# Kernel optimization log

Hardware: AMD Instinct MI355X
Metric: run time of the kernel (lower is better)

The kernel has to match this reference:

```python
import jax, jax.numpy as jnp
import numpy as np
import math

L = 4      # layers / experts
AD = 512   # agent dim per layer
D = 512    # wsi_size / model dim
T = 64     # num_tokens
N = 4096   # WSI patches
NC = 2
PROJ = 256 # cosine gate projection dim
HID = 4 * D
CAP = math.ceil(T / L)  # top-1, capacity_factor=1.0
EPS = 1e-5
AUX_W = 0.01


def layer_norm(x, g, b):
    x32 = x.astype(jnp.float32)
    mu = x32.mean(-1, keepdims=True)
    var = x32.var(-1, keepdims=True)
    return ((x32 - mu) * jax.lax.rsqrt(var + EPS) * g + b).astype(x.dtype)


def mha(q_in, kv_in, w_qkv, b_qkv, w_out, b_out, n_heads):
    # torch nn.MultiheadAttention, unbatched (len, embed) inputs
    E = q_in.shape[-1]
    hd = E // n_heads
    wq, wk, wv = jnp.split(w_qkv, 3, axis=0)
    bq, bk, bv = jnp.split(b_qkv, 3)
    q = (q_in @ wq.T + bq).reshape(-1, n_heads, hd)
    k = (kv_in @ wk.T + bk).reshape(-1, n_heads, hd)
    v = (kv_in @ wv.T + bv).reshape(-1, n_heads, hd)
    scale = float(1.0 / np.sqrt(hd))
    attn = jax.nn.softmax(jnp.einsum('thd,shd->hts', q, k) * scale, axis=-1)
    out = jnp.einsum('hts,shd->thd', attn, v).reshape(-1, E)
    return out @ w_out.T + b_out


def moe_top1(x, proj_w, sim_mat, temp, w1, b1, w2, b2):
    # tutel cosine top-1 gate (fp32), capacity-limited batch-prioritized dispatch
    E = w1.shape[0]
    xf = x.astype(jnp.float32)
    p = xf @ proj_w                                             # [T, PROJ]
    p = p / (jnp.linalg.norm(p, axis=-1, keepdims=True) + 1e-8)
    s = sim_mat / (jnp.linalg.norm(sim_mat, axis=0, keepdims=True) + 1e-8)
    scale = jnp.exp(jnp.minimum(temp, jnp.log(jnp.float32(100.0))))
    logits = (p @ s) * scale                                    # [T, E]
    scores = jax.nn.softmax(logits, axis=-1)
    expert = jnp.argmax(logits, axis=-1)                        # [T]
    gate = jnp.take_along_axis(scores, expert[:, None], axis=1)[:, 0]
    # batch prioritized routing: higher-gate tokens claim capacity slots first
    order = jnp.argsort(-gate)
    oh = jax.nn.one_hot(expert[order], E, dtype=jnp.int32)
    pos_s = jnp.sum(jnp.cumsum(oh, axis=0) * oh, axis=1) - 1    # slot within expert
    inv = jnp.argsort(order)
    pos = pos_s[inv]
    keep = pos < CAP
    safe_pos = jnp.where(keep, pos, 0)
    # dispatch -> grouped expert FFN -> combine
    buf = jnp.zeros((E, CAP, x.shape[-1]), x.dtype)
    buf = buf.at[expert, safe_pos].add(jnp.where(keep[:, None], x, 0.0))
    h = jax.nn.gelu(jnp.einsum('ecd,edh->ech', buf, w1) + b1[:, None, :], approximate=False)
    y = jnp.einsum('ech,ehd->ecd', h, w2) + b2[:, None, :]
    out = y[expert, safe_pos] * (gate * keep)[:, None].astype(x.dtype)
    # load-balancing aux loss (top-1)
    me = scores.mean(0)
    ce = jax.nn.one_hot(expert, E, dtype=jnp.float32).mean(0)
    l_aux = jnp.sum(me * ce) * E
    return out, l_aux


def reference(share_feature, fet_tokens, ind_ln1_g, ind_ln1_b, ind_ln2_g, ind_ln2_b,
              ind_qkv_w, ind_qkv_b, ind_out_w, ind_out_b, ind_mlp_w, ind_mlp_b,
              gate_proj_w, gate_sim, gate_temp, exp_w1, exp_b1, exp_w2, exp_b2,
              gsa_ln1_g, gsa_ln1_b, gsa_qkv_w, gsa_qkv_b, gsa_out_w, gsa_out_b,
              gsa_ln2_g, gsa_ln2_b, gsa_fc_w, gsa_fc_b, gsa_proj_w, gsa_proj_b,
              butter_w, butter_b, cls_w, cls_b):
    cur = jnp.zeros((T, D), share_feature.dtype)
    feature1 = jnp.zeros((L, T, D), share_feature.dtype)
    aux = jnp.zeros((1,), jnp.float32)
    for i in range(L):  # small fixed per-layer loop (structurally distinct params)
        seg = share_feature[:, i * AD:(i + 1) * AD]
        sf = layer_norm(seg, ind_ln1_g[i], ind_ln1_b[i])
        tok = layer_norm(fet_tokens[i], ind_ln2_g[i], ind_ln2_b[i])
        attn_out = mha(tok, sf, ind_qkv_w[i], ind_qkv_b[i], ind_out_w[i], ind_out_b[i], AD)
        qf = attn_out @ ind_mlp_w[i].T + ind_mlp_b[i]   # [T, D]
        mo, la = moe_top1(qf, gate_proj_w, gate_sim, gate_temp, exp_w1, exp_b1, exp_w2, exp_b2)
        cur = cur + mo
        aux = aux + la * AUX_W
        feature1 = feature1.at[i].set(cur)
    cur = cur / L
    # GatedSFAttentionBlock (8 heads self-attn + QuickGELU MLP, pre-LN residual)
    x1 = layer_norm(cur, gsa_ln1_g, gsa_ln1_b)
    x = cur + mha(x1, x1, gsa_qkv_w, gsa_qkv_b, gsa_out_w, gsa_out_b, D // 64)
    x2 = layer_norm(x, gsa_ln2_g, gsa_ln2_b)
    h = x2 @ gsa_fc_w.T + gsa_fc_b
    h = h * jax.nn.sigmoid(1.702 * h)  # QuickGELU
    gated = x + (h @ gsa_proj_w.T + gsa_proj_b)
    # OutputBlock
    hb = (gated @ butter_w.T + butter_b).reshape(1, -1)  # [1, T*256]
    logits = hb @ cls_w.T + cls_b                        # [1, NC]
    Y_hat = jnp.argmax(logits, axis=1, keepdims=True)
    hazards = jax.nn.sigmoid(logits)
    feature2 = jnp.zeros((L, T, D), share_feature.dtype)
    feature2_pre = jnp.zeros((L, 1, NC), share_feature.dtype)
    return (logits, hazards, Y_hat, aux, feature1, feature2, feature2_pre)


def setup_inputs() -> dict:
    key = jax.random.key(0)
    ks = iter(jax.random.split(key, 40))
    def rn(shape, scale=0.02):
        return scale * jax.random.normal(next(ks), shape, dtype=jnp.float32)
    return dict(
        share_feature=jax.random.normal(next(ks), (N, L * AD), dtype=jnp.float32),
        fet_tokens=rn((L, T, AD), AD ** -0.5),
        ind_ln1_g=jnp.ones((L, AD)), ind_ln1_b=jnp.zeros((L, AD)),
        ind_ln2_g=jnp.ones((L, AD)), ind_ln2_b=jnp.zeros((L, AD)),
        ind_qkv_w=rn((L, 3 * AD, AD)), ind_qkv_b=jnp.zeros((L, 3 * AD)),
        ind_out_w=rn((L, AD, AD)), ind_out_b=jnp.zeros((L, AD)),
        ind_mlp_w=rn((L, D, AD)), ind_mlp_b=jnp.zeros((L, D)),
        gate_proj_w=rn((D, PROJ)), gate_sim=rn((PROJ, L)),
        gate_temp=jnp.asarray(np.log(10.0), jnp.float32),
        exp_w1=rn((L, D, HID)), exp_b1=jnp.zeros((L, HID)),
        exp_w2=rn((L, HID, D)), exp_b2=jnp.zeros((L, D)),
        gsa_ln1_g=jnp.ones((D,)), gsa_ln1_b=jnp.zeros((D,)),
        gsa_qkv_w=rn((3 * D, D)), gsa_qkv_b=jnp.zeros((3 * D,)),
        gsa_out_w=rn((D, D)), gsa_out_b=jnp.zeros((D,)),
        gsa_ln2_g=jnp.ones((D,)), gsa_ln2_b=jnp.zeros((D,)),
        gsa_fc_w=rn((4 * D, D)), gsa_fc_b=jnp.zeros((4 * D,)),
        gsa_proj_w=rn((D, 4 * D)), gsa_proj_b=jnp.zeros((D,)),
        butter_w=rn((256, D)), butter_b=jnp.zeros((256,)),
        cls_w=rn((NC, T * 256)), cls_b=jnp.zeros((NC,)),
    )
```

## Files before the change

### kernel.cpp

```cpp
#include <hip/hip_runtime.h>
#include <math.h>

#define LNUM 4
#define ADIM 512
#define TTOK 64
#define NSEQ 4096
#define HIDE 2048
#define CAPE 16
#define EPSV 1e-5f

typedef __bf16 bf16;
typedef bf16 bf16x8 __attribute__((ext_vector_type(8)));
typedef float f32x4 __attribute__((ext_vector_type(4)));

#define OFF_KT      0
#define OFF_VT      (OFF_KT   + LNUM*512*NSEQ)
#define OFF_KMAX    (OFF_VT   + LNUM*512*NSEQ)
#define OFF_KMIN    (OFF_KMAX + LNUM*512)
#define OFF_Q       (OFF_KMIN + LNUM*512)
#define OFF_AO      (OFF_Q    + LNUM*TTOK*512)
#define OFF_AP      (OFF_AO   + LNUM*TTOK*512)
#define OFF_QF      (OFF_AP   + LNUM*TTOK*512)
#define OFF_GATE    (OFF_QF   + LNUM*TTOK*512)
#define OFF_EXP     (OFF_GATE + LNUM*TTOK)
#define OFF_POS     (OFF_EXP  + LNUM*TTOK)
#define OFF_KEEP    (OFF_POS  + LNUM*TTOK)
#define OFF_BUF     (OFF_KEEP + LNUM*TTOK)
#define OFF_SSUM    (OFF_BUF  + LNUM*4*CAPE*512)
#define OFF_CNT     (OFF_SSUM + LNUM*4)
#define ZERO_N      (LNUM*4*CAPE*512 + LNUM*4 + LNUM*4)
#define OFF_HEXP    (OFF_CNT  + LNUM*4)
#define OFF_YEXP    (OFF_HEXP + LNUM*4*CAPE*HIDE)
#define OFF_CUR     (OFF_YEXP + LNUM*4*CAPE*512)
#define OFF_Q3      (OFF_CUR  + TTOK*512)
#define OFF_K3      (OFF_Q3   + TTOK*512)
#define OFF_V3      (OFF_K3   + TTOK*512)
#define OFF_AO2     (OFF_V3   + TTOK*512)
#define OFF_XB      (OFF_AO2  + TTOK*512)
#define OFF_HROW    (OFF_XB   + TTOK*512)
#define OFF_HB      (OFF_HROW + TTOK*HIDE)
#define OFF_GATED   (OFF_HB   + TTOK*256)
#define OFF_AH      (OFF_GATED + TTOK*512)
#define OFF_AL      (OFF_AH + LNUM*NSEQ*256)
#define OFF_WH      (OFF_AL + LNUM*NSEQ*256)
#define OFF_WL      (OFF_WH + LNUM*1024*256)

#define O_F1   6
#define O_F2   (6 + LNUM*TTOK*512)
#define O_F2P  (O_F2 + LNUM*TTOK*512)

__device__ __forceinline__ float wave_sum(float v) {
#pragma unroll
  for (int o = 32; o > 0; o >>= 1) v += __shfl_down(v, o, 64);
  return v;
}

__device__ __forceinline__ float block_sum256(float v) {
  __shared__ float r[4];
  v = wave_sum(v);
  int wid = threadIdx.x >> 6, lane = threadIdx.x & 63;
  if (lane == 0) r[wid] = v;
  __syncthreads();
  float s = r[0] + r[1] + r[2] + r[3];
  __syncthreads();
  return s;
}

__global__ void k_zero(float* __restrict__ p, int n) {
  int i = blockIdx.x * 256 + threadIdx.x;
  if (i < n) p[i] = 0.f;
}

__global__ __launch_bounds__(64) void k_cvt_a(const float* __restrict__ SF,
      const float* __restrict__ G, const float* __restrict__ Bta,
      bf16* __restrict__ AH, bf16* __restrict__ AL) {
  int row = blockIdx.x;
  int l = row >> 12, m = row & 4095;
  int lane = threadIdx.x;
  const float* src = SF + (size_t)m * (LNUM * ADIM) + l * ADIM;
  float4 a = *(const float4*)(src + lane * 8);
  float4 b = *(const float4*)(src + lane * 8 + 4);
  float sum = (a.x + a.y) + (a.z + a.w) + (b.x + b.y) + (b.z + b.w);
  float sq = a.x*a.x + a.y*a.y + a.z*a.z + a.w*a.w + b.x*b.x + b.y*b.y + b.z*b.z + b.w*b.w;
  sum = wave_sum(sum); sq = wave_sum(sq);
  sum = __shfl(sum, 0, 64); sq = __shfl(sq, 0, 64);
  float mu = sum * (1.f / 512.f);
  float rs = rsqrtf(sq * (1.f / 512.f) - mu * mu + EPSV);
  float4 g0 = *(const float4*)(G + l * 512 + lane * 8);
  float4 g1 = *(const float4*)(G + l * 512 + lane * 8 + 4);
  float4 c0 = *(const float4*)(Bta + l * 512 + lane * 8);
  float4 c1 = *(const float4*)(Bta + l * 512 + lane * 8 + 4);
  float x[8];
  x[0] = (a.x - mu) * rs * g0.x + c0.x;  x[1] = (a.y - mu) * rs * g0.y + c0.y;
  x[2] = (a.z - mu) * rs * g0.z + c0.z;  x[3] = (a.w - mu) * rs * g0.w + c0.w;
  x[4] = (b.x - mu) * rs * g1.x + c1.x;  x[5] = (b.y - mu) * rs * g1.y + c1.y;
  x[6] = (b.z - mu) * rs * g1.z + c1.z;  x[7] = (b.w - mu) * rs * g1.w + c1.w;
  bf16x8 vh, vl;
#pragma unroll
  for (int j = 0; j < 8; j++) {
    bf16 h = (bf16)x[j];
    vh[j] = h;
    vl[j] = (bf16)(x[j] - (float)h);
  }
  *(bf16x8*)(AH + (size_t)row * 512 + lane * 8) = vh;
  *(bf16x8*)(AL + (size_t)row * 512 + lane * 8) = vl;
}

__global__ __launch_bounds__(64) void k_cvt_w(const float* __restrict__ Wqkv,
      bf16* __restrict__ WH, bf16* __restrict__ WL) {
  int row = blockIdx.x;
  int l = row >> 10, r = row & 1023;
  int lane = threadIdx.x;
  const float* src = Wqkv + (size_t)l * 1536 * 512 + (size_t)(512 + r) * 512 + lane * 8;
  float4 a = *(const float4*)(src);
  float4 b = *(const float4*)(src + 4);
  float x[8] = {a.x, a.y, a.z, a.w, b.x, b.y, b.z, b.w};
  bf16x8 vh, vl;
#pragma unroll
  for (int j = 0; j < 8; j++) {
    bf16 h = (bf16)x[j];
    vh[j] = h;
    vl[j] = (bf16)(x[j] - (float)h);
  }
  *(bf16x8*)(WH + (size_t)row * 512 + lane * 8) = vh;
  *(bf16x8*)(WL + (size_t)row * 512 + lane * 8) = vl;
}

__global__ __launch_bounds__(256) void k_mfma_kv(
      const bf16* __restrict__ AH, const bf16* __restrict__ AL,
      const bf16* __restrict__ WH, const bf16* __restrict__ WL,
      const float* __restrict__ Bqkv,
      float* __restrict__ KT, float* __restrict__ VT) {
  __shared__ bf16 sAh[128*32], sAl[128*32], sWh[128*32], sWl[128*32];
  int l = blockIdx.z;
  int n0 = blockIdx.x * 128, m0 = blockIdx.y * 128;
  int tid = threadIdx.x;
  int lane = tid & 63;
  int w = tid >> 6;
  int wm = w >> 1, wn = w & 1;
  const bf16* gAh = AH + ((size_t)l * 4096 + m0) * 512;
  const bf16* gAl = AL + ((size_t)l * 4096 + m0) * 512;
  const bf16* gWh = WH + ((size_t)l * 1024 + n0) * 512;
  const bf16* gWl = WL + ((size_t)l * 1024 + n0) * 512;
  int ch0 = tid * 2, ch1 = tid * 2 + 1;
  int r0 = ch0 >> 2, q0 = (ch0 & 3) * 8;
  int r1 = ch1 >> 2, q1 = (ch1 & 3) * 8;
  int fr = lane & 15, fq = (lane >> 4) * 8;
  f32x4 acc[4][4] = {};
  for (int k0 = 0; k0 < 512; k0 += 32) {
    *(bf16x8*)&sAh[r0*32 + q0] = *(const bf16x8*)&gAh[(size_t)r0*512 + k0 + q0];
    *(bf16x8*)&sAh[r1*32 + q1] = *(const bf16x8*)&gAh[(size_t)r1*512 + k0 + q1];
    *(bf16x8*)&sAl[r0*32 + q0] = *(const bf16x8*)&gAl[(size_t)r0*512 + k0 + q0];
    *(bf16x8*)&sAl[r1*32 + q1] = *(const bf16x8*)&gAl[(size_t)r1*512 + k0 + q1];
    *(bf16x8*)&sWh[r0*32 + q0] = *(const bf16x8*)&gWh[(size_t)r0*512 + k0 + q0];
    *(bf16x8*)&sWh[r1*32 + q1] = *(const bf16x8*)&gWh[(size_t)r1*512 + k0 + q1];
    *(bf16x8*)&sWl[r0*32 + q0] = *(const bf16x8*)&gWl[(size_t)r0*512 + k0 + q0];
    *(bf16x8*)&sWl[r1*32 + q1] = *(const bf16x8*)&gWl[(size_t)r1*512 + k0 + q1];
    __syncthreads();
    bf16x8 ah[4], al[4], bh[4], bl[4];
#pragma unroll
    for (int i = 0; i < 4; i++) {
      ah[i] = *(const bf16x8*)&sAh[(wm*64 + i*16 + fr)*32 + fq];
      al[i] = *(const bf16x8*)&sAl[(wm*64 + i*16 + fr)*32 + fq];
      bh[i] = *(const bf16x8*)&sWh[(wn*64 + i*16 + fr)*32 + fq];
      bl[i] = *(const bf16x8*)&sWl[(wn*64 + i*16 + fr)*32 + fq];
    }
#pragma unroll
    for (int i = 0; i < 4; i++)
#pragma unroll
      for (int j = 0; j < 4; j++) {
        acc[i][j] = __builtin_amdgcn_mfma_f32_16x16x32_bf16(ah[i], bh[j], acc[i][j], 0, 0, 0);
        acc[i][j] = __builtin_amdgcn_mfma_f32_16x16x32_bf16(ah[i], bl[j], acc[i][j], 0, 0, 0);
        acc[i][j] = __builtin_amdgcn_mfma_f32_16x16x32_bf16(al[i], bh[j], acc[i][j], 0, 0, 0);
      }
    __syncthreads();
  }
#pragma unroll
  for (int j = 0; j < 4; j++) {
    int n = n0 + wn*64 + j*16 + fr;
    float bias = Bqkv[l * 1536 + 512 + n];
    float* base = (n < 512) ? (KT + ((size_t)(l*512 + n)) * 4096)
                            : (VT + ((size_t)(l*512 + n - 512)) * 4096);
#pragma unroll
    for (int i = 0; i < 4; i++) {
      int mb = m0 + wm*64 + i*16 + (lane >> 4) * 4;
      float4 o = make_float4(acc[i][j][0] + bias, acc[i][j][1] + bias,
                             acc[i][j][2] + bias, acc[i][j][3] + bias);
      *(float4*)(base + mb) = o;
    }
  }
}

__global__ __launch_bounds__(256) void k_minmax(const float* __restrict__ KT,
                                                float* __restrict__ kmax, float* __restrict__ kmin) {
  int row = blockIdx.x;
  const float4* k = (const float4*)(KT + (size_t)row * 4096);
  float mx = -3.4e38f, mn = 3.4e38f;
  for (int i = threadIdx.x; i < 1024; i += 256) {
    float4 v = k[i];
    mx = fmaxf(mx, fmaxf(fmaxf(v.x, v.y), fmaxf(v.z, v.w)));
    mn = fminf(mn, fminf(fminf(v.x, v.y), fminf(v.z, v.w)));
  }
#pragma unroll
  for (int o = 32; o > 0; o >>= 1) {
    mx = fmaxf(mx, __shfl_down(mx, o, 64));
    mn = fminf(mn, __shfl_down(mn, o, 64));
  }
  __shared__ float rmx[4], rmn[4];
  int wid = threadIdx.x >> 6, lane = threadIdx.x & 63;
  if (lane == 0) { rmx[wid] = mx; rmn[wid] = mn; }
  __syncthreads();
  if (threadIdx.x == 0) {
    kmax[row] = fmaxf(fmaxf(rmx[0], rmx[1]), fmaxf(rmx[2], rmx[3]));
    kmin[row] = fminf(fminf(rmn[0], rmn[1]), fminf(rmn[2], rmn[3]));
  }
}

__global__ __launch_bounds__(256) void k_q(const float* __restrict__ TOK,
      const float* __restrict__ G, const float* __restrict__ Bta,
      const float* __restrict__ Wqkv, const float* __restrict__ Bqkv,
      float* __restrict__ Q) {
  int t = blockIdx.x, l = blockIdx.y;
  int tid = threadIdx.x;
  __shared__ float xr[512];
  const float* x = TOK + ((size_t)l * TTOK + t) * ADIM;
  float v0 = x[tid], v1 = x[tid + 256];
  float sum = block_sum256(v0 + v1);
  float sq = block_sum256(v0 * v0 + v1 * v1);
  float m = sum * (1.f / 512.f);
  float rs = rsqrtf(sq * (1.f / 512.f) - m * m + EPSV);
  xr[tid]       = (v0 - m) * rs * G[l * 512 + tid] + Bta[l * 512 + tid];
  xr[tid + 256] = (v1 - m) * rs * G[l * 512 + tid + 256] + Bta[l * 512 + tid + 256];
  __syncthreads();
  int h = blockIdx.z * 256 + tid;
  const float4* w = (const float4*)(Wqkv + (size_t)l * 1536 * 512 + (size_t)h * 512);
  float acc = 0.f;
#pragma unroll 8
  for (int c = 0; c < 128; c++) {
    float4 wv = w[c]; float4 xv = ((const float4*)xr)[c];
    acc = fmaf(wv.x, xv.x, acc); acc = fmaf(wv.y, xv.y, acc);
    acc = fmaf(wv.z, xv.z, acc); acc = fmaf(wv.w, xv.w, acc);
  }
  Q[((size_t)l * TTOK + t) * 512 + h] = acc + Bqkv[l * 1536 + h];
}

__global__ __launch_bounds__(256) void k_attn(const float* __restrict__ KT, const float* __restrict__ VT,
      const float* __restrict__ Q, const float* __restrict__ kmax, const float* __restrict__ kmin,
      float* __restrict__ AO) {
  int h = blockIdx.x, l = blockIdx.y;
  int tid = threadIdx.x;
  int w = tid >> 6, lane = tid & 63;
  __shared__ float pden[4][64], pnum[4][64];
  size_t base = ((size_t)(l * 512 + h)) * 4096 + w * 1024;
  float kv[16], vv[16];
#pragma unroll
  for (int c = 0; c < 4; c++) {
    *(float4*)&kv[c*4] = *(const float4*)(KT + base + c * 256 + lane * 4);
    *(float4*)&vv[c*4] = *(const float4*)(VT + base + c * 256 + lane * 4);
  }
  float q_own = Q[((size_t)l * TTOK + lane) * 512 + h];
  float km = kmax[l * 512 + h], kn = kmin[l * 512 + h];
  for (int t = 0; t < 64; t++) {
    float qt = __shfl(q_own, t, 64);
    float mt = (qt >= 0.f) ? qt * km : qt * kn;
    float den = 0.f, num = 0.f;
#pragma unroll
    for (int i = 0; i < 16; i++) {
      float e = __expf(fmaf(qt, kv[i], -mt));
      den += e;
      num = fmaf(e, vv[i], num);
    }
#pragma unroll
    for (int o = 32; o > 0; o >>= 1) {
      den += __shfl_down(den, o, 64);
      num += __shfl_down(num, o, 64);
    }
    if (lane == 0) { pden[w][t] = den; pnum[w][t] = num; }
  }
  __syncthreads();
  if (w == 0) {
    float d = pden[0][lane] + pden[1][lane] + pden[2][lane] + pden[3][lane];
    float n = pnum[0][lane] + pnum[1][lane] + pnum[2][lane] + pnum[3][lane];
    AO[((size_t)l * TTOK + lane) * 512 + h] = n / d;
  }
}

__global__ __launch_bounds__(256) void k_rowgemm512(const float* __restrict__ IN,
      const float* __restrict__ W, const float* __restrict__ B, const float* __restrict__ RES,
      float* __restrict__ OUT, unsigned long long wsl, int bsl) {
  int t = blockIdx.x, l = blockIdx.y;
  int row = l * gridDim.x + t;
  int tid = threadIdx.x;
  const float4* xr = (const float4*)(IN + (size_t)row * 512);
  int h = blockIdx.z * 256 + tid;
  const float4* w = (const float4*)(W + (size_t)l * wsl + (size_t)h * 512);
  float acc = 0.f;
#pragma unroll 8
  for (int c = 0; c < 128; c++) {
    float4 wv = w[c]; float4 xv = xr[c];
    acc = fmaf(wv.x, xv.x, acc); acc = fmaf(wv.y, xv.y, acc);
    acc = fmaf(wv.z, xv.z, acc); acc = fmaf(wv.w, xv.w, acc);
  }
  float o = acc + B[l * bsl + h];
  if (RES) o += RES[(size_t)row * 512 + h];
  OUT[(size_t)row * 512 + h] = o;
}

__global__ __launch_bounds__(256) void k_gate(const float* __restrict__ QF,
      const float* __restrict__ PW, const float* __restrict__ SIM, const float* __restrict__ TEMP,
      float* __restrict__ gate, int* __restrict__ expert,
      float* __restrict__ ssum, int* __restrict__ cnt) {
  int t = blockIdx.x, l = blockIdx.y;
  int tid = threadIdx.x;
  __shared__ float sp[256];
  __shared__ float lg[4];
  const float* x = QF + ((size_t)l * TTOK + t) * 512;
  float p = 0.f;
  for (int c = 0; c < 512; c++) p = fmaf(x[c], PW[c * 256 + tid], p);
  float nrm = block_sum256(p * p);
  float pn = p / (sqrtf(nrm) + 1e-8f);
  sp[tid] = pn;
  __syncthreads();
  if (tid < 4) {
    float ls = 0.f, ns = 0.f;
    for (int j = 0; j < 256; j++) {
      float sv = SIM[j * 4 + tid];
      ls = fmaf(sp[j], sv, ls);
      ns = fmaf(sv, sv, ns);
    }
    float scale = __expf(fminf(TEMP[0], 4.6051701859880914f));
    lg[tid] = ls / (sqrtf(ns) + 1e-8f) * scale;
  }
  __syncthreads();
  if (tid == 0) {
    float l0 = lg[0], l1 = lg[1], l2 = lg[2], l3 = lg[3];
    int best = 0; float bv = l0;
    if (l1 > bv) { best = 1; bv = l1; }
    if (l2 > bv) { best = 2; bv = l2; }
    if (l3 > bv) { best = 3; bv = l3; }
    float mx = fmaxf(fmaxf(l0, l1), fmaxf(l2, l3));
    float e0 = __expf(l0 - mx), e1 = __expf(l1 - mx), e2 = __expf(l2 - mx), e3 = __expf(l3 - mx);
    float inv = 1.f / (e0 + e1 + e2 + e3);
    float s0 = e0 * inv, s1 = e1 * inv, s2 = e2 * inv, s3 = e3 * inv;
    float sb = (best == 0) ? s0 : (best == 1) ? s1 : (best == 2) ? s2 : s3;
    gate[l * TTOK + t] = sb;
    expert[l * TTOK + t] = best;
    atomicAdd(&ssum[l * 4 + 0], s0); atomicAdd(&ssum[l * 4 + 1], s1);
    atomicAdd(&ssum[l * 4 + 2], s2); atomicAdd(&ssum[l * 4 + 3], s3);
    atomicAdd(&cnt[l * 4 + best], 1);
  }
}

__global__ __launch_bounds__(64) void k_route(const float* __restrict__ gate, const int* __restrict__ expert,
                                              int* __restrict__ pos, int* __restrict__ keep) {
  int l = blockIdx.x;
  int t = threadIdx.x;
  __shared__ float g[64];
  __shared__ int e[64];
  g[t] = gate[l * TTOK + t]; e[t] = expert[l * TTOK + t];
  __syncthreads();
  float gt = g[t]; int et = e[t];
  int p = 0;
  for (int u = 0; u < 64; u++)
    if (e[u] == et && (g[u] > gt || (g[u] == gt && u < t))) p++;
  pos[l * TTOK + t] = p;
  keep[l * TTOK + t] = (p < CAPE) ? 1 : 0;
}

__global__ __launch_bounds__(128) void k_scatter(const float* __restrict__ QF, const int* __restrict__ expert,
      const int* __restrict__ pos, const int* __restrict__ keep, float* __restrict__ buf) {
  int t = blockIdx.x, l = blockIdx.y;
  int idx = l * TTOK + t;
  if (!keep[idx]) return;
  int e = expert[idx], p = pos[idx];
  const float4* src = (const float4*)(QF + ((size_t)l * TTOK + t) * 512);
  float4* dst = (float4*)(buf + (((size_t)(l * 4 + e)) * CAPE + p) * 512);
  dst[threadIdx.x] = src[threadIdx.x];
}

__global__ __launch_bounds__(256) void k_moe_h(const float* __restrict__ buf, const float* __restrict__ W1,
      const float* __restrict__ B1, float* __restrict__ H) {
  int le = blockIdx.y;
  int e = le & 3;
  int col = blockIdx.x * 256 + threadIdx.x;
  const float* act = buf + (size_t)le * 16 * 512;
  const float* wp = W1 + (size_t)e * 512 * HIDE + col;
  float acc[16];
#pragma unroll
  for (int c = 0; c < 16; c++) acc[c] = 0.f;
  for (int k0 = 0; k0 < 512; k0 += 4) {
    float4 a[16];
#pragma unroll
    for (int c = 0; c < 16; c++) a[c] = *(const float4*)(act + c * 512 + k0);
#pragma unroll
    for (int j = 0; j < 4; j++) {
      float wv = wp[(size_t)(k0 + j) * HIDE];
#pragma unroll
      for (int c = 0; c < 16; c++) acc[c] = fmaf(((const float*)&a[c])[j], wv, acc[c]);
    }
  }
  float bias = B1[e * HIDE + col];
  float* outp = H + (size_t)le * 16 * HIDE + col;
#pragma unroll
  for (int c = 0; c < 16; c++) {
    float v = acc[c] + bias;
    outp[(size_t)c * HIDE] = 0.5f * v * (1.f + erff(v * 0.70710678118654752f));
  }
}

__global__ __launch_bounds__(256) void k_moe_y(const float* __restrict__ H, const float* __restrict__ W2,
      const float* __restrict__ B2, float* __restrict__ Y) {
  int le = blockIdx.y;
  int e = le & 3;
  int cl = threadIdx.x & 63, kq = threadIdx.x >> 6;
  int col = blockIdx.x * 64 + cl;
  const float* act = H + (size_t)le * 16 * HIDE + kq * 512;
  const float* wp = W2 + (size_t)e * HIDE * 512 + (size_t)(kq * 512) * 512 + col;
  float acc[16];
#pragma unroll
  for (int c = 0; c < 16; c++) acc[c] = 0.f;
  for (int k0 = 0; k0 < 512; k0 += 4) {
    float4 a[16];
#pragma unroll
    for (int c = 0; c < 16; c++) a[c] = *(const float4*)(act + c * HIDE + k0);
#pragma unroll
    for (int j = 0; j < 4; j++) {
      float wv = wp[(size_t)(k0 + j) * 512];
#pragma unroll
      for (int c = 0; c < 16; c++) acc[c] = fmaf(((const float*)&a[c])[j], wv, acc[c]);
    }
  }
  __shared__ float sacc[4][16][64];
#pragma unroll
  for (int c = 0; c < 16; c++) sacc[kq][c][cl] = acc[c];
  __syncthreads();
  if (kq == 0) {
    float bias = B2[e * 512 + col];
#pragma unroll
    for (int c = 0; c < 16; c++) {
      float tot = sacc[0][c][cl] + sacc[1][c][cl] + sacc[2][c][cl] + sacc[3][c][cl] + bias;
      Y[(size_t)le * 16 * 512 + (size_t)c * 512 + col] = tot;
    }
  }
}

__global__ __launch_bounds__(512) void k_combine(const float* __restrict__ Y, const int* __restrict__ expert,
      const int* __restrict__ pos, const int* __restrict__ keep, const float* __restrict__ gate,
      float* __restrict__ f1, float* __restrict__ f2, float* __restrict__ cur) {
  int t = blockIdx.x;
  int d = threadIdx.x;
  float acc = 0.f;
#pragma unroll
  for (int l = 0; l < LNUM; l++) {
    int idx = l * TTOK + t;
    float v = 0.f;
    if (keep[idx]) {
      int e = expert[idx], p = pos[idx];
      v = Y[(((size_t)(l * 4 + e)) * CAPE + p) * 512 + d] * gate[idx];
    }
    acc += v;
    f1[((size_t)l * TTOK + t) * 512 + d] = acc;
    f2[((size_t)l * TTOK + t) * 512 + d] = 0.f;
  }
  cur[(size_t)t * 512 + d] = acc * 0.25f;
}

__global__ __launch_bounds__(256) void k_gsa_qkv(const float* __restrict__ CUR,
      const float* __restrict__ G, const float* __restrict__ Bta,
      const float* __restrict__ W, const float* __restrict__ B,
      float* __restrict__ Q3, float* __restrict__ K3, float* __restrict__ V3) {
  int t = blockIdx.x;
  int tid = threadIdx.x;
  __shared__ float xr[512];
  const float* x = CUR + (size_t)t * 512;
  float v0 = x[tid], v1 = x[tid + 256];
  float sum = block_sum256(v0 + v1);
  float sq = block_sum256(v0 * v0 + v1 * v1);
  float m = sum * (1.f / 512.f);
  float rs = rsqrtf(sq * (1.f / 512.f) - m * m + EPSV);
  xr[tid] = (v0 - m) * rs * G[tid] + Bta[tid];
  xr[tid + 256] = (v1 - m) * rs * G[tid + 256] + Bta[tid + 256];
  __syncthreads();
  int h = blockIdx.y * 256 + tid;
  const float4* w = (const float4*)(W + (size_t)h * 512);
  float acc = 0.f;
#pragma unroll 8
  for (int c = 0; c < 128; c++) {
    float4 wv = w[c]; float4 xv = ((const float4*)xr)[c];
    acc = fmaf(wv.x, xv.x, acc); acc = fmaf(wv.y, xv.y, acc);
    acc = fmaf(wv.z, xv.z, acc); acc = fmaf(wv.w, xv.w, acc);
  }
  float o = acc + B[h];
  if (h < 512) Q3[(size_t)t * 512 + h] = o;
  else if (h < 1024) K3[(size_t)t * 512 + (h - 512)] = o;
  else V3[(size_t)t * 512 + (h - 1024)] = o;
}

__global__ __launch_bounds__(256) void k_gsa_attn(const float* __restrict__ Q3, const float* __restrict__ K3,
      const float* __restrict__ V3, float* __restrict__ AO2) {
  int h = blockIdx.x;
  __shared__ float qh[64][65], kh[64][65], vh[64][65];
  __shared__ float ps[4][64];
  for (int i = threadIdx.x; i < 4096; i += 256) {
    int t = i >> 6, d = i & 63;
    qh[t][d] = Q3[(size_t)t * 512 + h * 64 + d];
    kh[t][d] = K3[(size_t)t * 512 + h * 64 + d];
    vh[t][d] = V3[(size_t)t * 512 + h * 64 + d];
  }
  __syncthreads();
  int w = threadIdx.x >> 6, lane = threadIdx.x & 63;
  for (int tt = 0; tt < 16; tt++) {
    int t = w * 16 + tt;
    float acc = 0.f;
#pragma unroll 8
    for (int d = 0; d < 64; d++) acc = fmaf(qh[t][d], kh[lane][d], acc);
    acc *= 0.125f;
    float m = acc;
#pragma unroll
    for (int o = 32; o > 0; o >>= 1) m = fmaxf(m, __shfl_xor(m, o, 64));
    float e = __expf(acc - m);
    float den = e;
#pragma unroll
    for (int o = 32; o > 0; o >>= 1) den += __shfl_xor(den, o, 64);
    ps[w][lane] = e / den;
    __syncthreads();
    float o2 = 0.f;
#pragma unroll 8
    for (int s = 0; s < 64; s++) o2 = fmaf(ps[w][s], vh[s][lane], o2);
    AO2[(size_t)t * 512 + h * 64 + lane] = o2;
    __syncthreads();
  }
}

__global__ __launch_bounds__(256) void k_gsa_fc(const float* __restrict__ XB,
      const float* __restrict__ G, const float* __restrict__ Bta,
      const float* __restrict__ W, const float* __restrict__ B, float* __restrict__ H) {
  int t = blockIdx.x;
  int tid = threadIdx.x;
  __shared__ float xr[512];
  const float* x = XB + (size_t)t * 512;
  float v0 = x[tid], v1 = x[tid + 256];
  float sum = block_sum256(v0 + v1);
  float sq = block_sum256(v0 * v0 + v1 * v1);
  float m = sum * (1.f / 512.f);
  float rs = rsqrtf(sq * (1.f / 512.f) - m * m + EPSV);
  xr[tid] = (v0 - m) * rs * G[tid] + Bta[tid];
  xr[tid + 256] = (v1 - m) * rs * G[tid + 256] + Bta[tid + 256];
  __syncthreads();
  int o = blockIdx.y * 256 + tid;
  const float4* w = (const float4*)(W + (size_t)o * 512);
  float acc = 0.f;
#pragma unroll 8
  for (int c = 0; c < 128; c++) {
    float4 wv = w[c]; float4 xv = ((const float4*)xr)[c];
    acc = fmaf(wv.x, xv.x, acc); acc = fmaf(wv.y, xv.y, acc);
    acc = fmaf(wv.z, xv.z, acc); acc = fmaf(wv.w, xv.w, acc);
  }
  acc += B[o];
  H[(size_t)t * HIDE + o] = acc / (1.f + __expf(-1.702f * acc));
}

__global__ __launch_bounds__(256) void k_gsa_gated(const float* __restrict__ XB, const float* __restrict__ HROW,
      const float* __restrict__ PW, const float* __restrict__ PB, float* __restrict__ GATED) {
  int t = blockIdx.x;
  int tid = threadIdx.x;
  const float4* hp = (const float4*)(HROW + (size_t)t * HIDE);
  int o = blockIdx.y * 256 + tid;
  const float4* w = (const float4*)(PW + (size_t)o * HIDE);
  float acc = 0.f;
#pragma unroll 4
  for (int c = 0; c < 512; c++) {
    float4 wv = w[c]; float4 xv = hp[c];
    acc = fmaf(wv.x, xv.x, acc); acc = fmaf(wv.y, xv.y, acc);
    acc = fmaf(wv.z, xv.z, acc); acc = fmaf(wv.w, xv.w, acc);
  }
  GATED[(size_t)t * 512 + o] = acc + PB[o] + XB[(size_t)t * 512 + o];
}

__global__ __launch_bounds__(256) void k_butter(const float* __restrict__ GATED,
      const float* __restrict__ BW, const float* __restrict__ BB, float* __restrict__ HB) {
  int t = blockIdx.x;
  int tid = threadIdx.x;
  const float4* gr = (const float4*)(GATED + (size_t)t * 512);
  const float4* w = (const float4*)(BW + (size_t)tid * 512);
  float acc = 0.f;
#pragma unroll 8
  for (int c = 0; c < 128; c++) {
    float4 wv = w[c]; float4 xv = gr[c];
    acc = fmaf(wv.x, xv.x, acc); acc = fmaf(wv.y, xv.y, acc);
    acc = fmaf(wv.z, xv.z, acc); acc = fmaf(wv.w, xv.w, acc);
  }
  HB[(size_t)t * 256 + tid] = acc + BB[tid];
}

__global__ __launch_bounds__(256) void k_final(const float* __restrict__ HB,
      const float* __restrict__ CW, const float* __restrict__ CB,
      const float* __restrict__ ssum, const int* __restrict__ cnt,
      float* __restrict__ out) {
  int tid = threadIdx.x;
  float p0 = 0.f, p1 = 0.f;
  for (int i = tid; i < 16384; i += 256) {
    float h = HB[i];
    p0 = fmaf(h, CW[i], p0);
    p1 = fmaf(h, CW[16384 + i], p1);
  }
  p0 = block_sum256(p0);
  p1 = block_sum256(p1);
  if (tid == 0) {
    float l0 = p0 + CB[0], l1 = p1 + CB[1];
    out[0] = l0; out[1] = l1;
    out[2] = 1.f / (1.f + __expf(-l0));
    out[3] = 1.f / (1.f + __expf(-l1));
    out[4] = (l1 > l0) ? 1.f : 0.f;
    float aux = 0.f;
    for (int i = 0; i < 16; i++) aux += (ssum[i] * (1.f / 64.f)) * ((float)cnt[i] * (1.f / 64.f));
    out[5] = aux * 4.f * 0.01f;
  }
  if (tid < 8) out[O_F2P + tid] = 0.f;
}

extern "C" void kernel_launch(void* const* d_in, const int* in_sizes, int n_in,
                              void* d_out, int out_size, void* d_ws, size_t ws_size,
                              hipStream_t stream) {
  const float* SF    = (const float*)d_in[0];
  const float* TOK   = (const float*)d_in[1];
  const float* LN1G  = (const float*)d_in[2];
  const float* LN1B  = (const float*)d_in[3];
  const float* LN2G  = (const float*)d_in[4];
  const float* LN2B  = (const float*)d_in[5];
  const float* QKVW  = (const float*)d_in[6];
  const float* QKVB  = (const float*)d_in[7];
  const float* OUTW  = (const float*)d_in[8];
  const float* OUTB  = (const float*)d_in[9];
  const float* MLPW  = (const float*)d_in[10];
  const float* MLPB  = (const float*)d_in[11];
  const float* GPW   = (const float*)d_in[12];
  const float* GSIM  = (const float*)d_in[13];
  const float* GTMP  = (const float*)d_in[14];
  const float* EW1   = (const float*)d_in[15];
  const float* EB1   = (const float*)d_in[16];
  const float* EW2   = (const float*)d_in[17];
  const float* EB2   = (const float*)d_in[18];
  const float* GL1G  = (const float*)d_in[19];
  const float* GL1B  = (const float*)d_in[20];
  const float* GQKVW = (const float*)d_in[21];
  const float* GQKVB = (const float*)d_in[22];
  const float* GOUTW = (const float*)d_in[23];
  const float* GOUTB = (const float*)d_in[24];
  const float* GL2G  = (const float*)d_in[25];
  const float* GL2B  = (const float*)d_in[26];
  const float* GFCW  = (const float*)d_in[27];
  const float* GFCB  = (const float*)d_in[28];
  const float* GPJW  = (const float*)d_in[29];
  const float* GPJB  = (const float*)d_in[30];
  const float* BTW   = (const float*)d_in[31];
  const float* BTB   = (const float*)d_in[32];
  const float* CLW   = (const float*)d_in[33];
  const float* CLB   = (const float*)d_in[34];

  float* ws  = (float*)d_ws;
  float* out = (float*)d_out;

  float* KT   = ws + OFF_KT;
  float* VT   = ws + OFF_VT;
  float* KMAX = ws + OFF_KMAX;
  float* KMIN = ws + OFF_KMIN;
  float* Q    = ws + OFF_Q;
  float* AO   = ws + OFF_AO;
  float* AP   = ws + OFF_AP;
  float* QF   = ws + OFF_QF;
  float* GATE = ws + OFF_GATE;
  int*   EXPI = (int*)(ws + OFF_EXP);
  int*   POSI = (int*)(ws + OFF_POS);
  int*   KEEPI= (int*)(ws + OFF_KEEP);
  float* BUF  = ws + OFF_BUF;
  float* SSUM = ws + OFF_SSUM;
  int*   CNT  = (int*)(ws + OFF_CNT);
  float* HEXP = ws + OFF_HEXP;
  float* YEXP = ws + OFF_YEXP;
  float* CUR  = ws + OFF_CUR;
  float* Q3   = ws + OFF_Q3;
  float* K3   = ws + OFF_K3;
  float* V3   = ws + OFF_V3;
  float* AO2  = ws + OFF_AO2;
  float* XB   = ws + OFF_XB;
  float* HROW = ws + OFF_HROW;
  float* HBB  = ws + OFF_HB;
  float* GTD  = ws + OFF_GATED;
  bf16*  AH   = (bf16*)(ws + OFF_AH);
  bf16*  AL   = (bf16*)(ws + OFF_AL);
  bf16*  WH   = (bf16*)(ws + OFF_WH);
  bf16*  WL   = (bf16*)(ws + OFF_WL);

  k_zero<<<(ZERO_N + 255) / 256, 256, 0, stream>>>(BUF, ZERO_N);
  k_cvt_a<<<LNUM * NSEQ, 64, 0, stream>>>(SF, LN1G, LN1B, AH, AL);
  k_cvt_w<<<LNUM * 1024, 64, 0, stream>>>(QKVW, WH, WL);
  k_mfma_kv<<<dim3(8, 32, LNUM), 256, 0, stream>>>(AH, AL, WH, WL, QKVB, KT, VT);
  k_minmax<<<LNUM * 512, 256, 0, stream>>>(KT, KMAX, KMIN);
  k_q<<<dim3(TTOK, LNUM, 2), 256, 0, stream>>>(TOK, LN2G, LN2B, QKVW, QKVB, Q);
  k_attn<<<dim3(512, LNUM), 256, 0, stream>>>(KT, VT, Q, KMAX, KMIN, AO);
  k_rowgemm512<<<dim3(TTOK, LNUM, 2), 256, 0, stream>>>(AO, OUTW, OUTB, nullptr, AP, 512ull * 512ull, 512);
  k_rowgemm512<<<dim3(TTOK, LNUM, 2), 256, 0, stream>>>(AP, MLPW, MLPB, nullptr, QF, 512ull * 512ull, 512);
  k_gate<<<dim3(TTOK, LNUM), 256, 0, stream>>>(QF, GPW, GSIM, GTMP, GATE, EXPI, SSUM, CNT);
  k_route<<<LNUM, 64, 0, stream>>>(GATE, EXPI, POSI, KEEPI);
  k_scatter<<<dim3(TTOK, LNUM), 128, 0, stream>>>(QF, EXPI, POSI, KEEPI, BUF);
  k_moe_h<<<dim3(8, 16), 256, 0, stream>>>(BUF, EW1, EB1, HEXP);
  k_moe_y<<<dim3(8, 16), 256, 0, stream>>>(HEXP, EW2, EB2, YEXP);
  k_combine<<<TTOK, 512, 0, stream>>>(YEXP, EXPI, POSI, KEEPI, GATE, out + O_F1, out + O_F2, CUR);
  k_gsa_qkv<<<dim3(TTOK, 6), 256, 0, stream>>>(CUR, GL1G, GL1B, GQKVW, GQKVB, Q3, K3, V3);
  k_gsa_attn<<<8, 256, 0, stream>>>(Q3, K3, V3, AO2);
  k_rowgemm512<<<dim3(TTOK, 1, 2), 256, 0, stream>>>(AO2, GOUTW, GOUTB, CUR, XB, 0ull, 0);
  k_gsa_fc<<<dim3(TTOK, 8), 256, 0, stream>>>(XB, GL2G, GL2B, GFCW, GFCB, HROW);
  k_gsa_gated<<<dim3(TTOK, 2), 256, 0, stream>>>(XB, HROW, GPJW, GPJB, GTD);
  k_butter<<<TTOK, 256, 0, stream>>>(GTD, BTW, BTB, HBB);
  k_final<<<1, 256, 0, stream>>>(HBB, CLW, CLB, SSUM, CNT, out);
}
```

Baseline: 945.9 us.

## Replace per-row GEMV kernels with tiled split-K SGEMM using atomic accumulation

Replaces the row-at-a-time matrix-vector kernels for the small 64-token projections (Q, out-proj, MLP, gate projection, GSA qkv/fc/proj, butter) with a shared-memory tiled 64x64 GEMM. It splits K across blocks and accumulates into zero-initialised outputs with atomicAdd, so each weight tile is loaded once per 64 tokens instead of once per token. LayerNorm and swish move into separate small kernels, and the workspace is reordered so every atomic target sits in the zeroed region. The attention kernel is restructured so each thread handles one query and streams K/V itself instead of doing per-token wave reductions. The atomics make results order-dependent, and the extra launches add overhead.

```diff
diff --git a/kernel.cpp b/kernel.cpp
--- a/kernel.cpp
+++ b/kernel.cpp
@@ -13,37 +13,36 @@
 typedef bf16 bf16x8 __attribute__((ext_vector_type(8)));
 typedef float f32x4 __attribute__((ext_vector_type(4)));
 
-#define OFF_KT      0
-#define OFF_VT      (OFF_KT   + LNUM*512*NSEQ)
-#define OFF_KMAX    (OFF_VT   + LNUM*512*NSEQ)
-#define OFF_KMIN    (OFF_KMAX + LNUM*512)
-#define OFF_Q       (OFF_KMIN + LNUM*512)
-#define OFF_AO      (OFF_Q    + LNUM*TTOK*512)
-#define OFF_AP      (OFF_AO   + LNUM*TTOK*512)
-#define OFF_QF      (OFF_AP   + LNUM*TTOK*512)
-#define OFF_GATE    (OFF_QF   + LNUM*TTOK*512)
-#define OFF_EXP     (OFF_GATE + LNUM*TTOK)
-#define OFF_POS     (OFF_EXP  + LNUM*TTOK)
-#define OFF_KEEP    (OFF_POS  + LNUM*TTOK)
-#define OFF_BUF     (OFF_KEEP + LNUM*TTOK)
-#define OFF_SSUM    (OFF_BUF  + LNUM*4*CAPE*512)
-#define OFF_CNT     (OFF_SSUM + LNUM*4)
-#define ZERO_N      (LNUM*4*CAPE*512 + LNUM*4 + LNUM*4)
-#define OFF_HEXP    (OFF_CNT  + LNUM*4)
-#define OFF_YEXP    (OFF_HEXP + LNUM*4*CAPE*HIDE)
-#define OFF_CUR     (OFF_YEXP + LNUM*4*CAPE*512)
-#define OFF_Q3      (OFF_CUR  + TTOK*512)
-#define OFF_K3      (OFF_Q3   + TTOK*512)
-#define OFF_V3      (OFF_K3   + TTOK*512)
-#define OFF_AO2     (OFF_V3   + TTOK*512)
-#define OFF_XB      (OFF_AO2  + TTOK*512)
-#define OFF_HROW    (OFF_XB   + TTOK*512)
-#define OFF_HB      (OFF_HROW + TTOK*HIDE)
-#define OFF_GATED   (OFF_HB   + TTOK*256)
-#define OFF_AH      (OFF_GATED + TTOK*512)
-#define OFF_AL      (OFF_AH + LNUM*NSEQ*256)
-#define OFF_WH      (OFF_AL + LNUM*NSEQ*256)
-#define OFF_WL      (OFF_WH + LNUM*1024*256)
+#define OFF_BUF   0
+#define OFF_SSUM  (OFF_BUF  + 131072)
+#define OFF_CNT   (OFF_SSUM + 16)
+#define OFF_Q     (OFF_CNT  + 16)
+#define OFF_AP    (OFF_Q    + 131072)
+#define OFF_QF    (OFF_AP   + 131072)
+#define OFF_P     (OFF_QF   + 131072)
+#define OFF_QKV3  (OFF_P    + 65536)
+#define OFF_XB    (OFF_QKV3 + 98304)
+#define OFF_HROW  (OFF_XB   + 32768)
+#define OFF_GTD   (OFF_HROW + 131072)
+#define OFF_HB    (OFF_GTD  + 32768)
+#define ZERO_N    (OFF_HB   + 16384)
+#define OFF_KT    ZERO_N
+#define OFF_VT    (OFF_KT   + LNUM*512*NSEQ)
+#define OFF_KMAX  (OFF_VT   + LNUM*512*NSEQ)
+#define OFF_KMIN  (OFF_KMAX + LNUM*512)
+#define OFF_AO    (OFF_KMIN + LNUM*512)
+#define OFF_GATE  (OFF_AO   + 131072)
+#define OFF_EXP   (OFF_GATE + 256)
+#define OFF_POS   (OFF_EXP  + 256)
+#define OFF_KEEP  (OFF_POS  + 256)
+#define OFF_HEXP  (OFF_KEEP + 256)
+#define OFF_CUR   (OFF_HEXP + LNUM*4*CAPE*HIDE)
+#define OFF_AO2   (OFF_CUR  + TTOK*512)
+#define OFF_AH    (OFF_AO2  + TTOK*512)
+#define OFF_AL    (OFF_AH + LNUM*NSEQ*256)
+#define OFF_WH    (OFF_AL + LNUM*NSEQ*256)
+#define OFF_WL    (OFF_WH + LNUM*1024*256)
+#define OFF_YEXP  OFF_AH
 
 #define O_F1   6
 #define O_F2   (6 + LNUM*TTOK*512)
@@ -54,7 +53,11 @@
   for (int o = 32; o > 0; o >>= 1) v += __shfl_down(v, o, 64);
   return v;
 }
-
+__device__ __forceinline__ float wave_sum_all(float v) {
+#pragma unroll
+  for (int o = 32; o > 0; o >>= 1) v += __shfl_xor(v, o, 64);
+  return v;
+}
 __device__ __forceinline__ float block_sum256(float v) {
   __shared__ float r[4];
   v = wave_sum(v);
@@ -82,8 +85,7 @@
   float4 b = *(const float4*)(src + lane * 8 + 4);
   float sum = (a.x + a.y) + (a.z + a.w) + (b.x + b.y) + (b.z + b.w);
   float sq = a.x*a.x + a.y*a.y + a.z*a.z + a.w*a.w + b.x*b.x + b.y*b.y + b.z*b.z + b.w*b.w;
-  sum = wave_sum(sum); sq = wave_sum(sq);
-  sum = __shfl(sum, 0, 64); sq = __shfl(sq, 0, 64);
+  sum = wave_sum_all(sum); sq = wave_sum_all(sq);
   float mu = sum * (1.f / 512.f);
   float rs = rsqrtf(sq * (1.f / 512.f) - mu * mu + EPSV);
   float4 g0 = *(const float4*)(G + l * 512 + lane * 8);
@@ -216,32 +218,128 @@
   }
 }
 
-__global__ __launch_bounds__(256) void k_q(const float* __restrict__ TOK,
-      const float* __restrict__ G, const float* __restrict__ Bta,
-      const float* __restrict__ Wqkv, const float* __restrict__ Bqkv,
-      float* __restrict__ Q) {
+__global__ __launch_bounds__(64) void k_ln(const float* __restrict__ IN,
+      const float* __restrict__ G, const float* __restrict__ B,
+      float* __restrict__ OUT, int gstride) {
   int t = blockIdx.x, l = blockIdx.y;
+  int row = l * 64 + t;
+  int lane = threadIdx.x;
+  const float* x = IN + (size_t)row * 512 + lane * 8;
+  float4 a = ((const float4*)x)[0], b = ((const float4*)x)[1];
+  float sum = (a.x + a.y) + (a.z + a.w) + (b.x + b.y) + (b.z + b.w);
+  float sq = a.x*a.x + a.y*a.y + a.z*a.z + a.w*a.w + b.x*b.x + b.y*b.y + b.z*b.z + b.w*b.w;
+  sum = wave_sum_all(sum); sq = wave_sum_all(sq);
+  float mu = sum * (1.f / 512.f);
+  float rs = rsqrtf(sq * (1.f / 512.f) - mu * mu + EPSV);
+  const float* gp = G + l * gstride + lane * 8;
+  const float* bp = B + l * gstride + lane * 8;
+  float4 g0 = ((const float4*)gp)[0], g1 = ((const float4*)gp)[1];
+  float4 c0 = ((const float4*)bp)[0], c1 = ((const float4*)bp)[1];
+  float4 o0, o1;
+  o0.x = (a.x - mu) * rs * g0.x + c0.x;  o0.y = (a.y - mu) * rs * g0.y + c0.y;
+  o0.z = (a.z - mu) * rs * g0.z + c0.z;  o0.w = (a.w - mu) * rs * g0.w + c0.w;
+  o1.x = (b.x - mu) * rs * g1.x + c1.x;  o1.y = (b.y - mu) * rs * g1.y + c1.y;
+  o1.z = (b.z - mu) * rs * g1.z + c1.z;  o1.w = (b.w - mu) * rs * g1.w + c1.w;
+  float* op = OUT + (size_t)row * 512 + lane * 8;
+  ((float4*)op)[0] = o0; ((float4*)op)[1] = o1;
+}
+
+__global__ __launch_bounds__(256) void k_gemm64(
+      const float* __restrict__ IN, const float* __restrict__ W,
+      const float* __restrict__ BIAS, const float* __restrict__ RES,
+      float* __restrict__ OUT, int K, int N, long wl, int bl) {
+  int l = blockIdx.z;
+  int n0 = blockIdx.x * 64;
+  int kc0 = blockIdx.y * 128;
+  const float* INl = IN + (size_t)l * 64 * K;
+  const float* Wl  = W + (size_t)l * wl;
+  float* OUTl = OUT + (size_t)l * 64 * N;
+  __shared__ float sA[64][68], sB[64][68];
   int tid = threadIdx.x;
-  __shared__ float xr[512];
-  const float* x = TOK + ((size_t)l * TTOK + t) * ADIM;
-  float v0 = x[tid], v1 = x[tid + 256];
-  float sum = block_sum256(v0 + v1);
-  float sq = block_sum256(v0 * v0 + v1 * v1);
-  float m = sum * (1.f / 512.f);
-  float rs = rsqrtf(sq * (1.f / 512.f) - m * m + EPSV);
-  xr[tid]       = (v0 - m) * rs * G[l * 512 + tid] + Bta[l * 512 + tid];
-  xr[tid + 256] = (v1 - m) * rs * G[l * 512 + tid + 256] + Bta[l * 512 + tid + 256];
-  __syncthreads();
-  int h = blockIdx.z * 256 + tid;
-  const float4* w = (const float4*)(Wqkv + (size_t)l * 1536 * 512 + (size_t)h * 512);
-  float acc = 0.f;
+  int tx = tid & 15, ty = tid >> 4;
+  float acc[4][4];
+  if (blockIdx.y == 0) {
+#pragma unroll
+    for (int j = 0; j < 4; j++) {
+      float bv = BIAS ? BIAS[bl * l + n0 + tx*4 + j] : 0.f;
+#pragma unroll
+      for (int i = 0; i < 4; i++)
+        acc[i][j] = bv + (RES ? RES[((size_t)l*64 + ty*4 + i) * N + n0 + tx*4 + j] : 0.f);
+    }
+  } else {
+#pragma unroll
+    for (int i = 0; i < 4; i++)
+#pragma unroll
+      for (int j = 0; j < 4; j++) acc[i][j] = 0.f;
+  }
+  for (int kc = kc0; kc < kc0 + 128; kc += 64) {
+    for (int i = tid; i < 1024; i += 256) {
+      int r = i >> 4;
+      int kq = i & 15;
+      float4 av = *(const float4*)(INl + (size_t)r * K + kc + kq*4);
+      sA[kq*4+0][r] = av.x; sA[kq*4+1][r] = av.y; sA[kq*4+2][r] = av.z; sA[kq*4+3][r] = av.w;
+      float4 bv = *(const float4*)(Wl + (size_t)(n0 + r) * K + kc + kq*4);
+      sB[kq*4+0][r] = bv.x; sB[kq*4+1][r] = bv.y; sB[kq*4+2][r] = bv.z; sB[kq*4+3][r] = bv.w;
+    }
+    __syncthreads();
 #pragma unroll 8
-  for (int c = 0; c < 128; c++) {
-    float4 wv = w[c]; float4 xv = ((const float4*)xr)[c];
-    acc = fmaf(wv.x, xv.x, acc); acc = fmaf(wv.y, xv.y, acc);
-    acc = fmaf(wv.z, xv.z, acc); acc = fmaf(wv.w, xv.w, acc);
-  }
-  Q[((size_t)l * TTOK + t) * 512 + h] = acc + Bqkv[l * 1536 + h];
+    for (int kk = 0; kk < 64; kk++) {
+      float4 a4 = *(const float4*)&sA[kk][ty*4];
+      float4 b4 = *(const float4*)&sB[kk][tx*4];
+      float a[4] = {a4.x,a4.y,a4.z,a4.w}, b[4] = {b4.x,b4.y,b4.z,b4.w};
+#pragma unroll
+      for (int i = 0; i < 4; i++)
+#pragma unroll
+        for (int j = 0; j < 4; j++) acc[i][j] = fmaf(a[i], b[j], acc[i][j]);
+    }
+    __syncthreads();
+  }
+#pragma unroll
+  for (int i = 0; i < 4; i++)
+#pragma unroll
+    for (int j = 0; j < 4; j++)
+      atomicAdd(&OUTl[(size_t)(ty*4+i) * N + n0 + tx*4 + j], acc[i][j]);
+}
+
+__global__ __launch_bounds__(256) void k_gemm64t(
+      const float* __restrict__ IN, const float* __restrict__ W,
+      float* __restrict__ OUT, int K, int N) {
+  int l = blockIdx.z;
+  int n0 = blockIdx.x * 64;
+  int kc0 = blockIdx.y * 128;
+  const float* INl = IN + (size_t)l * 64 * K;
+  float* OUTl = OUT + (size_t)l * 64 * N;
+  __shared__ float sA[64][68], sB[64][68];
+  int tid = threadIdx.x;
+  int tx = tid & 15, ty = tid >> 4;
+  float acc[4][4] = {};
+  for (int kc = kc0; kc < kc0 + 128; kc += 64) {
+    for (int i = tid; i < 1024; i += 256) {
+      int r = i >> 4;
+      int kq = i & 15;
+      float4 av = *(const float4*)(INl + (size_t)r * K + kc + kq*4);
+      sA[kq*4+0][r] = av.x; sA[kq*4+1][r] = av.y; sA[kq*4+2][r] = av.z; sA[kq*4+3][r] = av.w;
+      float4 bv = *(const float4*)(W + (size_t)(kc + r) * N + n0 + kq*4);
+      *(float4*)&sB[r][kq*4] = bv;
+    }
+    __syncthreads();
+#pragma unroll 8
+    for (int kk = 0; kk < 64; kk++) {
+      float4 a4 = *(const float4*)&sA[kk][ty*4];
+      float4 b4 = *(const float4*)&sB[kk][tx*4];
+      float a[4] = {a4.x,a4.y,a4.z,a4.w}, b[4] = {b4.x,b4.y,b4.z,b4.w};
+#pragma unroll
+      for (int i = 0; i < 4; i++)
+#pragma unroll
+        for (int j = 0; j < 4; j++) acc[i][j] = fmaf(a[i], b[j], acc[i][j]);
+    }
+    __syncthreads();
+  }
+#pragma unroll
+  for (int i = 0; i < 4; i++)
+#pragma unroll
+    for (int j = 0; j < 4; j++)
+      atomicAdd(&OUTl[(size_t)(ty*4+i) * N + n0 + tx*4 + j], acc[i][j]);
 }
 
 __global__ __launch_bounds__(256) void k_attn(const float* __restrict__ KT, const float* __restrict__ VT,
@@ -249,105 +347,77 @@
       float* __restrict__ AO) {
   int h = blockIdx.x, l = blockIdx.y;
   int tid = threadIdx.x;
-  int w = tid >> 6, lane = tid & 63;
+  int w = tid >> 6, t = tid & 63;
   __shared__ float pden[4][64], pnum[4][64];
-  size_t base = ((size_t)(l * 512 + h)) * 4096 + w * 1024;
-  float kv[16], vv[16];
-#pragma unroll
-  for (int c = 0; c < 4; c++) {
-    *(float4*)&kv[c*4] = *(const float4*)(KT + base + c * 256 + lane * 4);
-    *(float4*)&vv[c*4] = *(const float4*)(VT + base + c * 256 + lane * 4);
-  }
-  float q_own = Q[((size_t)l * TTOK + lane) * 512 + h];
+  const float* kp = KT + ((size_t)(l * 512 + h)) * 4096 + w * 1024;
+  const float* vp = VT + ((size_t)(l * 512 + h)) * 4096 + w * 1024;
+  float q = Q[((size_t)l * TTOK + t) * 512 + h];
   float km = kmax[l * 512 + h], kn = kmin[l * 512 + h];
-  for (int t = 0; t < 64; t++) {
-    float qt = __shfl(q_own, t, 64);
-    float mt = (qt >= 0.f) ? qt * km : qt * kn;
-    float den = 0.f, num = 0.f;
-#pragma unroll
-    for (int i = 0; i < 16; i++) {
-      float e = __expf(fmaf(qt, kv[i], -mt));
-      den += e;
-      num = fmaf(e, vv[i], num);
-    }
-#pragma unroll
-    for (int o = 32; o > 0; o >>= 1) {
-      den += __shfl_down(den, o, 64);
-      num += __shfl_down(num, o, 64);
-    }
-    if (lane == 0) { pden[w][t] = den; pnum[w][t] = num; }
-  }
+  float m = (q >= 0.f) ? q * km : q * kn;
+  float d0 = 0.f, d1 = 0.f, n0 = 0.f, n1 = 0.f;
+  for (int s = 0; s < 1024; s += 8) {
+    float4 ka = *(const float4*)(kp + s), kb = *(const float4*)(kp + s + 4);
+    float4 va = *(const float4*)(vp + s), vb = *(const float4*)(vp + s + 4);
+    float e;
+    e = __expf(fmaf(q, ka.x, -m)); d0 += e; n0 = fmaf(e, va.x, n0);
+    e = __expf(fmaf(q, ka.y, -m)); d1 += e; n1 = fmaf(e, va.y, n1);
+    e = __expf(fmaf(q, ka.z, -m)); d0 += e; n0 = fmaf(e, va.z, n0);
+    e = __expf(fmaf(q, ka.w, -m)); d1 += e; n1 = fmaf(e, va.w, n1);
+    e = __expf(fmaf(q, kb.x, -m)); d0 += e; n0 = fmaf(e, vb.x, n0);
+    e = __expf(fmaf(q, kb.y, -m)); d1 += e; n1 = fmaf(e, vb.y, n1);
+    e = __expf(fmaf(q, kb.z, -m)); d0 += e; n0 = fmaf(e, vb.z, n0);
+    e = __expf(fmaf(q, kb.w, -m)); d1 += e; n1 = fmaf(e, vb.w, n1);
+  }
+  pden[w][t] = d0 + d1; pnum[w][t] = n0 + n1;
   __syncthreads();
   if (w == 0) {
-    float d = pden[0][lane] + pden[1][lane] + pden[2][lane] + pden[3][lane];
-    float n = pnum[0][lane] + pnum[1][lane] + pnum[2][lane] + pnum[3][lane];
-    AO[((size_t)l * TTOK + lane) * 512 + h] = n / d;
-  }
-}
-
-__global__ __launch_bounds__(256) void k_rowgemm512(const float* __restrict__ IN,
-      const float* __restrict__ W, const float* __restrict__ B, const float* __restrict__ RES,
-      float* __restrict__ OUT, unsigned long long wsl, int bsl) {
-  int t = blockIdx.x, l = blockIdx.y;
-  int row = l * gridDim.x + t;
-  int tid = threadIdx.x;
-  const float4* xr = (const float4*)(IN + (size_t)row * 512);
-  int h = blockIdx.z * 256 + tid;
-  const float4* w = (const float4*)(W + (size_t)l * wsl + (size_t)h * 512);
-  float acc = 0.f;
-#pragma unroll 8
-  for (int c = 0; c < 128; c++) {
-    float4 wv = w[c]; float4 xv = xr[c];
-    acc = fmaf(wv.x, xv.x, acc); acc = fmaf(wv.y, xv.y, acc);
-    acc = fmaf(wv.z, xv.z, acc); acc = fmaf(wv.w, xv.w, acc);
-  }
-  float o = acc + B[l * bsl + h];
-  if (RES) o += RES[(size_t)row * 512 + h];
-  OUT[(size_t)row * 512 + h] = o;
-}
-
-__global__ __launch_bounds__(256) void k_gate(const float* __restrict__ QF,
-      const float* __restrict__ PW, const float* __restrict__ SIM, const float* __restrict__ TEMP,
+    float d = pden[0][t] + pden[1][t] + pden[2][t] + pden[3][t];
+    float n = pnum[0][t] + pnum[1][t] + pnum[2][t] + pnum[3][t];
+    AO[((size_t)l * TTOK + t) * 512 + h] = n / d;
+  }
+}
+
+__global__ __launch_bounds__(64) void k_gate2(const float* __restrict__ P,
+      const float* __restrict__ SIM, const float* __restrict__ TEMP,
       float* __restrict__ gate, int* __restrict__ expert,
       float* __restrict__ ssum, int* __restrict__ cnt) {
   int t = blockIdx.x, l = blockIdx.y;
-  int tid = threadIdx.x;
-  __shared__ float sp[256];
-  __shared__ float lg[4];
-  const float* x = QF + ((size_t)l * TTOK + t) * 512;
-  float p = 0.f;
-  for (int c = 0; c < 512; c++) p = fmaf(x[c], PW[c * 256 + tid], p);
-  float nrm = block_sum256(p * p);
-  float pn = p / (sqrtf(nrm) + 1e-8f);
-  sp[tid] = pn;
-  __syncthreads();
-  if (tid < 4) {
-    float ls = 0.f, ns = 0.f;
-    for (int j = 0; j < 256; j++) {
-      float sv = SIM[j * 4 + tid];
-      ls = fmaf(sp[j], sv, ls);
-      ns = fmaf(sv, sv, ns);
-    }
+  int lane = threadIdx.x;
+  float4 p4 = *(const float4*)(P + ((size_t)(l * 64 + t)) * 256 + lane * 4);
+  float ss = p4.x*p4.x + p4.y*p4.y + p4.z*p4.z + p4.w*p4.w;
+  ss = wave_sum_all(ss);
+  float invp = 1.f / (sqrtf(ss) + 1e-8f);
+  float le[4] = {}, ne[4] = {};
+#pragma unroll
+  for (int j = 0; j < 4; j++) {
+    float pv = (j == 0) ? p4.x : (j == 1) ? p4.y : (j == 2) ? p4.z : p4.w;
+    float4 s4 = *(const float4*)(SIM + (size_t)(lane * 4 + j) * 4);
+    le[0] = fmaf(pv, s4.x, le[0]); le[1] = fmaf(pv, s4.y, le[1]);
+    le[2] = fmaf(pv, s4.z, le[2]); le[3] = fmaf(pv, s4.w, le[3]);
+    ne[0] = fmaf(s4.x, s4.x, ne[0]); ne[1] = fmaf(s4.y, s4.y, ne[1]);
+    ne[2] = fmaf(s4.z, s4.z, ne[2]); ne[3] = fmaf(s4.w, s4.w, ne[3]);
+  }
+#pragma unroll
+  for (int e = 0; e < 4; e++) { le[e] = wave_sum_all(le[e]); ne[e] = wave_sum_all(ne[e]); }
+  if (lane == 0) {
     float scale = __expf(fminf(TEMP[0], 4.6051701859880914f));
-    lg[tid] = ls / (sqrtf(ns) + 1e-8f) * scale;
-  }
-  __syncthreads();
-  if (tid == 0) {
-    float l0 = lg[0], l1 = lg[1], l2 = lg[2], l3 = lg[3];
-    int best = 0; float bv = l0;
-    if (l1 > bv) { best = 1; bv = l1; }
-    if (l2 > bv) { best = 2; bv = l2; }
-    if (l3 > bv) { best = 3; bv = l3; }
-    float mx = fmaxf(fmaxf(l0, l1), fmaxf(l2, l3));
-    float e0 = __expf(l0 - mx), e1 = __expf(l1 - mx), e2 = __expf(l2 - mx), e3 = __expf(l3 - mx);
+    float lg[4];
+#pragma unroll
+    for (int e = 0; e < 4; e++) lg[e] = le[e] * invp / (sqrtf(ne[e]) + 1e-8f) * scale;
+    int best = 0; float bv = lg[0];
+    if (lg[1] > bv) { best = 1; bv = lg[1]; }
+    if (lg[2] > bv) { best = 2; bv = lg[2]; }
+    if (lg[3] > bv) { best = 3; bv = lg[3]; }
+    float mx = fmaxf(fmaxf(lg[0], lg[1]), fmaxf(lg[2], lg[3]));
+    float e0 = __expf(lg[0]-mx), e1 = __expf(lg[1]-mx), e2 = __expf(lg[2]-mx), e3 = __expf(lg[3]-mx);
     float inv = 1.f / (e0 + e1 + e2 + e3);
-    float s0 = e0 * inv, s1 = e1 * inv, s2 = e2 * inv, s3 = e3 * inv;
+    float s0 = e0*inv, s1 = e1*inv, s2 = e2*inv, s3 = e3*inv;
     float sb = (best == 0) ? s0 : (best == 1) ? s1 : (best == 2) ? s2 : s3;
     gate[l * TTOK + t] = sb;
     expert[l * TTOK + t] = best;
-    atomicAdd(&ssum[l * 4 + 0], s0); atomicAdd(&ssum[l * 4 + 1], s1);
-    atomicAdd(&ssum[l * 4 + 2], s2); atomicAdd(&ssum[l * 4 + 3], s3);
-    atomicAdd(&cnt[l * 4 + best], 1);
+    atomicAdd(&ssum[l*4+0], s0); atomicAdd(&ssum[l*4+1], s1);
+    atomicAdd(&ssum[l*4+2], s2); atomicAdd(&ssum[l*4+3], s3);
+    atomicAdd(&cnt[l*4+best], 1);
   }
 }
 
@@ -465,47 +535,15 @@
   cur[(size_t)t * 512 + d] = acc * 0.25f;
 }
 
-__global__ __launch_bounds__(256) void k_gsa_qkv(const float* __restrict__ CUR,
-      const float* __restrict__ G, const float* __restrict__ Bta,
-      const float* __restrict__ W, const float* __restrict__ B,
-      float* __restrict__ Q3, float* __restrict__ K3, float* __restrict__ V3) {
-  int t = blockIdx.x;
-  int tid = threadIdx.x;
-  __shared__ float xr[512];
-  const float* x = CUR + (size_t)t * 512;
-  float v0 = x[tid], v1 = x[tid + 256];
-  float sum = block_sum256(v0 + v1);
-  float sq = block_sum256(v0 * v0 + v1 * v1);
-  float m = sum * (1.f / 512.f);
-  float rs = rsqrtf(sq * (1.f / 512.f) - m * m + EPSV);
-  xr[tid] = (v0 - m) * rs * G[tid] + Bta[tid];
-  xr[tid + 256] = (v1 - m) * rs * G[tid + 256] + Bta[tid + 256];
-  __syncthreads();
-  int h = blockIdx.y * 256 + tid;
-  const float4* w = (const float4*)(W + (size_t)h * 512);
-  float acc = 0.f;
-#pragma unroll 8
-  for (int c = 0; c < 128; c++) {
-    float4 wv = w[c]; float4 xv = ((const float4*)xr)[c];
-    acc = fmaf(wv.x, xv.x, acc); acc = fmaf(wv.y, xv.y, acc);
-    acc = fmaf(wv.z, xv.z, acc); acc = fmaf(wv.w, xv.w, acc);
-  }
-  float o = acc + B[h];
-  if (h < 512) Q3[(size_t)t * 512 + h] = o;
-  else if (h < 1024) K3[(size_t)t * 512 + (h - 512)] = o;
-  else V3[(size_t)t * 512 + (h - 1024)] = o;
-}
-
-__global__ __launch_bounds__(256) void k_gsa_attn(const float* __restrict__ Q3, const float* __restrict__ K3,
-      const float* __restrict__ V3, float* __restrict__ AO2) {
+__global__ __launch_bounds__(256) void k_gsa_attn(const float* __restrict__ QKV3, float* __restrict__ AO2) {
   int h = blockIdx.x;
   __shared__ float qh[64][65], kh[64][65], vh[64][65];
   __shared__ float ps[4][64];
   for (int i = threadIdx.x; i < 4096; i += 256) {
     int t = i >> 6, d = i & 63;
-    qh[t][d] = Q3[(size_t)t * 512 + h * 64 + d];
-    kh[t][d] = K3[(size_t)t * 512 + h * 64 + d];
-    vh[t][d] = V3[(size_t)t * 512 + h * 64 + d];
+    qh[t][d] = QKV3[(size_t)t * 1536 + h * 64 + d];
+    kh[t][d] = QKV3[(size_t)t * 1536 + 512 + h * 64 + d];
+    vh[t][d] = QKV3[(size_t)t * 1536 + 1024 + h * 64 + d];
   }
   __syncthreads();
   int w = threadIdx.x >> 6, lane = threadIdx.x & 63;
@@ -532,65 +570,10 @@
   }
 }
 
-__global__ __launch_bounds__(256) void k_gsa_fc(const float* __restrict__ XB,
-      const float* __restrict__ G, const float* __restrict__ Bta,
-      const float* __restrict__ W, const float* __restrict__ B, float* __restrict__ H) {
-  int t = blockIdx.x;
-  int tid = threadIdx.x;
-  __shared__ float xr[512];
-  const float* x = XB + (size_t)t * 512;
-  float v0 = x[tid], v1 = x[tid + 256];
-  float sum = block_sum256(v0 + v1);
-  float sq = block_sum256(v0 * v0 + v1 * v1);
-  float m = sum * (1.f / 512.f);
-  float rs = rsqrtf(sq * (1.f / 512.f) - m * m + EPSV);
-  xr[tid] = (v0 - m) * rs * G[tid] + Bta[tid];
-  xr[tid + 256] = (v1 - m) * rs * G[tid + 256] + Bta[tid + 256];
-  __syncthreads();
-  int o = blockIdx.y * 256 + tid;
-  const float4* w = (const float4*)(W + (size_t)o * 512);
-  float acc = 0.f;
-#pragma unroll 8
-  for (int c = 0; c < 128; c++) {
-    float4 wv = w[c]; float4 xv = ((const float4*)xr)[c];
-    acc = fmaf(wv.x, xv.x, acc); acc = fmaf(wv.y, xv.y, acc);
-    acc = fmaf(wv.z, xv.z, acc); acc = fmaf(wv.w, xv.w, acc);
-  }
-  acc += B[o];
-  H[(size_t)t * HIDE + o] = acc / (1.f + __expf(-1.702f * acc));
-}
-
-__global__ __launch_bounds__(256) void k_gsa_gated(const float* __restrict__ XB, const float* __restrict__ HROW,
-      const float* __restrict__ PW, const float* __restrict__ PB, float* __restrict__ GATED) {
-  int t = blockIdx.x;
-  int tid = threadIdx.x;
-  const float4* hp = (const float4*)(HROW + (size_t)t * HIDE);
-  int o = blockIdx.y * 256 + tid;
-  const float4* w = (const float4*)(PW + (size_t)o * HIDE);
-  float acc = 0.f;
-#pragma unroll 4
-  for (int c = 0; c < 512; c++) {
-    float4 wv = w[c]; float4 xv = hp[c];
-    acc = fmaf(wv.x, xv.x, acc); acc = fmaf(wv.y, xv.y, acc);
-    acc = fmaf(wv.z, xv.z, acc); acc = fmaf(wv.w, xv.w, acc);
-  }
-  GATED[(size_t)t * 512 + o] = acc + PB[o] + XB[(size_t)t * 512 + o];
-}
-
-__global__ __launch_bounds__(256) void k_butter(const float* __restrict__ GATED,
-      const float* __restrict__ BW, const float* __restrict__ BB, float* __restrict__ HB) {
-  int t = blockIdx.x;
-  int tid = threadIdx.x;
-  const float4* gr = (const float4*)(GATED + (size_t)t * 512);
-  const float4* w = (const float4*)(BW + (size_t)tid * 512);
-  float acc = 0.f;
-#pragma unroll 8
-  for (int c = 0; c < 128; c++) {
-    float4 wv = w[c]; float4 xv = gr[c];
-    acc = fmaf(wv.x, xv.x, acc); acc = fmaf(wv.y, xv.y, acc);
-    acc = fmaf(wv.z, xv.z, acc); acc = fmaf(wv.w, xv.w, acc);
-  }
-  HB[(size_t)t * 256 + tid] = acc + BB[tid];
+__global__ __launch_bounds__(256) void k_swish(float* __restrict__ H) {
+  int i = blockIdx.x * 256 + threadIdx.x;
+  float x = H[i];
+  H[i] = x / (1.f + __expf(-1.702f * x));
 }
 
 __global__ __launch_bounds__(256) void k_final(const float* __restrict__ HB,
@@ -661,57 +644,61 @@
   float* ws  = (float*)d_ws;
   float* out = (float*)d_out;
 
+  float* BUF  = ws + OFF_BUF;
+  float* SSUM = ws + OFF_SSUM;
+  int*   CNT  = (int*)(ws + OFF_CNT);
+  float* Q    = ws + OFF_Q;
+  float* AP   = ws + OFF_AP;
+  float* QF   = ws + OFF_QF;
+  float* P    = ws + OFF_P;
+  float* QKV3 = ws + OFF_QKV3;
+  float* XB   = ws + OFF_XB;
+  float* HROW = ws + OFF_HROW;
+  float* GTD  = ws + OFF_GTD;
+  float* HBB  = ws + OFF_HB;
   float* KT   = ws + OFF_KT;
   float* VT   = ws + OFF_VT;
   float* KMAX = ws + OFF_KMAX;
   float* KMIN = ws + OFF_KMIN;
-  float* Q    = ws + OFF_Q;
-  float* AO   = ws + OFF_AO;
-  float* AP   = ws + OFF_AP;
-  float* QF   = ws + OFF_QF;
+  float* AOSH = ws + OFF_AO;
   float* GATE = ws + OFF_GATE;
   int*   EXPI = (int*)(ws + OFF_EXP);
   int*   POSI = (int*)(ws + OFF_POS);
   int*   KEEPI= (int*)(ws + OFF_KEEP);
-  float* BUF  = ws + OFF_BUF;
-  float* SSUM = ws + OFF_SSUM;
-  int*   CNT  = (int*)(ws + OFF_CNT);
   float* HEXP = ws + OFF_HEXP;
-  float* YEXP = ws + OFF_YEXP;
   float* CUR  = ws + OFF_CUR;
-  float* Q3   = ws + OFF_Q3;
-  float* K3   = ws + OFF_K3;
-  float* V3   = ws + OFF_V3;
   float* AO2  = ws + OFF_AO2;
-  float* XB   = ws + OFF_XB;
-  float* HROW = ws + OFF_HROW;
-  float* HBB  = ws + OFF_HB;
-  float* GTD  = ws + OFF_GATED;
   bf16*  AH   = (bf16*)(ws + OFF_AH);
   bf16*  AL   = (bf16*)(ws + OFF_AL);
   bf16*  WH   = (bf16*)(ws + OFF_WH);
   bf16*  WL   = (bf16*)(ws + OFF_WL);
-
-  k_zero<<<(ZERO_N + 255) / 256, 256, 0, stream>>>(BUF, ZERO_N);
+  float* YEXP = ws + OFF_YEXP;
+
+  k_zero<<<(ZERO_N + 255) / 256, 256, 0, stream>>>(ws, ZERO_N);
   k_cvt_a<<<LNUM * NSEQ, 64, 0, stream>>>(SF, LN1G, LN1B, AH, AL);
   k_cvt_w<<<LNUM * 1024, 64, 0, stream>>>(QKVW, WH, WL);
   k_mfma_kv<<<dim3(8, 32, LNUM), 256, 0, stream>>>(AH, AL, WH, WL, QKVB, KT, VT);
   k_minmax<<<LNUM * 512, 256, 0, stream>>>(KT, KMAX, KMIN);
-  k_q<<<dim3(TTOK, LNUM, 2), 256, 0, stream>>>(TOK, LN2G, LN2B, QKVW, QKVB, Q);
-  k_attn<<<dim3(512, LNUM), 256, 0, stream>>>(KT, VT, Q, KMAX, KMIN, AO);
-  k_rowgemm512<<<dim3(TTOK, LNUM, 2), 256, 0, stream>>>(AO, OUTW, OUTB, nullptr, AP, 512ull * 512ull, 512);
-  k_rowgemm512<<<dim3(TTOK, LNUM, 2), 256, 0, stream>>>(AP, MLPW, MLPB, nullptr, QF, 512ull * 512ull, 512);
-  k_gate<<<dim3(TTOK, LNUM), 256, 0, stream>>>(QF, GPW, GSIM, GTMP, GATE, EXPI, SSUM, CNT);
+  k_ln<<<dim3(TTOK, LNUM), 64, 0, stream>>>(TOK, LN2G, LN2B, AOSH, 512);
+  k_gemm64<<<dim3(8, 4, LNUM), 256, 0, stream>>>(AOSH, QKVW, QKVB, nullptr, Q, 512, 512, 1536L*512, 1536);
+  k_attn<<<dim3(512, LNUM), 256, 0, stream>>>(KT, VT, Q, KMAX, KMIN, AOSH);
+  k_gemm64<<<dim3(8, 4, LNUM), 256, 0, stream>>>(AOSH, OUTW, OUTB, nullptr, AP, 512, 512, 512L*512, 512);
+  k_gemm64<<<dim3(8, 4, LNUM), 256, 0, stream>>>(AP, MLPW, MLPB, nullptr, QF, 512, 512, 512L*512, 512);
+  k_gemm64t<<<dim3(4, 4, LNUM), 256, 0, stream>>>(QF, GPW, P, 512, 256);
+  k_gate2<<<dim3(TTOK, LNUM), 64, 0, stream>>>(P, GSIM, GTMP, GATE, EXPI, SSUM, CNT);
   k_route<<<LNUM, 64, 0, stream>>>(GATE, EXPI, POSI, KEEPI);
   k_scatter<<<dim3(TTOK, LNUM), 128, 0, stream>>>(QF, EXPI, POSI, KEEPI, BUF);
   k_moe_h<<<dim3(8, 16), 256, 0, stream>>>(BUF, EW1, EB1, HEXP);
   k_moe_y<<<dim3(8, 16), 256, 0, stream>>>(HEXP, EW2, EB2, YEXP);
   k_combine<<<TTOK, 512, 0, stream>>>(YEXP, EXPI, POSI, KEEPI, GATE, out + O_F1, out + O_F2, CUR);
-  k_gsa_qkv<<<dim3(TTOK, 6), 256, 0, stream>>>(CUR, GL1G, GL1B, GQKVW, GQKVB, Q3, K3, V3);
-  k_gsa_attn<<<8, 256, 0, stream>>>(Q3, K3, V3, AO2);
-  k_rowgemm512<<<dim3(TTOK, 1, 2), 256, 0, stream>>>(AO2, GOUTW, GOUTB, CUR, XB, 0ull, 0);
-  k_gsa_fc<<<dim3(TTOK, 8), 256, 0, stream>>>(XB, GL2G, GL2B, GFCW, GFCB, HROW);
-  k_gsa_gated<<<dim3(TTOK, 2), 256, 0, stream>>>(XB, HROW, GPJW, GPJB, GTD);
-  k_butter<<<TTOK, 256, 0, stream>>>(GTD, BTW, BTB, HBB);
+  k_ln<<<dim3(TTOK, 1), 64, 0, stream>>>(CUR, GL1G, GL1B, AOSH, 0);
+  k_gemm64<<<dim3(24, 4, 1), 256, 0, stream>>>(AOSH, GQKVW, GQKVB, nullptr, QKV3, 512, 1536, 0, 0);
+  k_gsa_attn<<<8, 256, 0, stream>>>(QKV3, AO2);
+  k_gemm64<<<dim3(8, 4, 1), 256, 0, stream>>>(AO2, GOUTW, GOUTB, CUR, XB, 512, 512, 0, 0);
+  k_ln<<<dim3(TTOK, 1), 64, 0, stream>>>(XB, GL2G, GL2B, AOSH, 0);
+  k_gemm64<<<dim3(32, 4, 1), 256, 0, stream>>>(AOSH, GFCW, GFCB, nullptr, HROW, 512, 2048, 0, 0);
+  k_swish<<<(TTOK * HIDE) / 256, 256, 0, stream>>>(HROW);
+  k_gemm64<<<dim3(8, 16, 1), 256, 0, stream>>>(HROW, GPJW, GPJB, XB, GTD, 2048, 512, 0, 0);
+  k_gemm64<<<dim3(4, 4, 1), 256, 0, stream>>>(GTD, BTW, BTB, nullptr, HBB, 512, 256, 0, 0);
   k_final<<<1, 256, 0, stream>>>(HBB, CLW, CLB, SSUM, CNT, out);
 }
```

Measured after the change: 818.3 us. 13.5% less time.
